# Optimization experiments

Hardware: AMD Instinct MI355X
Metric: run time of the kernel (lower is better)

The kernel has to match this reference:

```python
import jax, jax.numpy as jnp
import numpy as np

B = 32          # batch
IN_C = 8        # in_channels
OUT_C = 8       # out_channels
K = 3           # kernel_size
PAD = 1         # padding
STRIDE = 1
MC = 32         # manifold_channels
H = W = 512


def setup_inputs() -> dict:
    key = jax.random.key(0)
    ks = jax.random.split(key, 8)
    s = 0.05
    return {
        "q": jax.random.normal(ks[0], (B, 1, 8, 8), jnp.float32),
        "x": jax.random.normal(ks[1], (B, IN_C, H, W), jnp.float32),
        # manifold conv1: Conv2d(1, MC, 8) -> weight [MC,1,8,8], bias [MC]
        "wm1": jax.random.normal(ks[2], (MC, 1, 8, 8), jnp.float32) * s,
        "bm1": jax.random.normal(ks[3], (MC,), jnp.float32) * s,
        # manifold conv2: Conv2d(MC, MC, 1) -> stored as [MC_out, MC_in]
        "wm2": jax.random.normal(ks[4], (MC, MC), jnp.float32) * s,
        "bm2": jnp.zeros((MC,), jnp.float32),
        # weight_transform: ConvTranspose2d(MC, OUT_C*IN_C, K) -> [MC, OUT_C*IN_C, K, K]
        "wt": jax.random.normal(ks[5], (MC, OUT_C * IN_C, K, K), jnp.float32) * s,
        "bt": jnp.zeros((OUT_C * IN_C,), jnp.float32),
        # bias_transform: Conv2d(MC, OUT_C, 1) -> [OUT_C, MC]
        "wb": jax.random.normal(ks[6], (OUT_C, MC), jnp.float32) * s,
        "bb": jnp.zeros((OUT_C,), jnp.float32),
    }


def reference(q, x, wm1, bm1, wm2, bm2, wt, bt, wb, bb):
    # ---- manifold: Conv2d(1,MC,8) on 8x8 input == full contraction -> [B, MC]
    m = jnp.einsum('bihw,cihw->bc', q, wm1) + bm1
    m = jax.nn.leaky_relu(m)                      # torch default slope 0.01
    m = m @ wm2.T + bm2                           # 1x1 conv on 1x1 map
    m = jax.nn.leaky_relu(m)
    # ---- weight_transform: ConvTranspose2d from 1x1 input -> [B, OUT_C*IN_C, K, K]
    w = jnp.einsum('bc,cokl->bokl', m, wt) + bt[None, :, None, None]
    w = w.reshape(B, OUT_C, IN_C, K, K)           # per-sample conv filters
    # ---- bias_transform: 1x1 conv -> per-sample bias [B, OUT_C]
    b = m @ wb.T + bb
    # ---- per-sample conv2d (== grouped conv with groups=batch)
    def per_sample_conv(xi, wi):
        # xi: [IN_C, H, W], wi: [OUT_C, IN_C, K, K]
        return jax.lax.conv_general_dilated(
            xi[None], wi,
            window_strides=(STRIDE, STRIDE),
            padding=[(PAD, PAD), (PAD, PAD)],
            dimension_numbers=('NCHW', 'OIHW', 'NCHW'))[0]
    y = jax.vmap(per_sample_conv)(x, w)           # [B, OUT_C, H, W]
    y = y + b[:, :, None, None]
    return y
```

## Files before the change

### kernel.cpp

```cpp
#include <hip/hip_runtime.h>
#include <hip/hip_bf16.h>

#define B_    32
#define IN_C  8
#define OUT_C 8
#define KK    3
#define MC    32
#define HH_   512
#define WW_   512

__global__ __launch_bounds__(576) void manifold_kernel(
    const float* __restrict__ q, const float* __restrict__ wm1,
    const float* __restrict__ bm1, const float* __restrict__ wm2,
    const float* __restrict__ bm2, const float* __restrict__ wt,
    const float* __restrict__ bt, const float* __restrict__ wb,
    const float* __restrict__ bb, float* __restrict__ F,
    float* __restrict__ bS)
{
    __shared__ float m1s[MC];
    __shared__ float m2s[MC];
    const int b = blockIdx.x;
    const int t = threadIdx.x;

    if (t < MC) {
        float s = 0.f;
        #pragma unroll 8
        for (int j = 0; j < 64; ++j)
            s += q[b * 64 + j] * wm1[t * 64 + j];
        s += bm1[t];
        m1s[t] = (s > 0.f) ? s : 0.01f * s;
    }
    __syncthreads();
    if (t < MC) {
        float s2 = 0.f;
        #pragma unroll
        for (int k = 0; k < MC; ++k)
            s2 += m1s[k] * wm2[t * MC + k];
        s2 += bm2[t];
        m2s[t] = (s2 > 0.f) ? s2 : 0.01f * s2;
    }
    __syncthreads();

    {
        const int o   = t & 7;
        const int tap = t >> 3;
        const int i   = tap / 9;
        const int kk  = tap - i * 9;
        const int widx = (o * IN_C + i) * 9 + kk;
        float acc = bt[o * IN_C + i];
        #pragma unroll
        for (int cc = 0; cc < MC; ++cc)
            acc += m2s[cc] * wt[cc * 576 + widx];
        F[b * 576 + t] = acc;
    }

    if (t < OUT_C) {
        float acc = bb[t];
        #pragma unroll
        for (int cc = 0; cc < MC; ++cc)
            acc += m2s[cc] * wb[t * MC + cc];
        bS[b * OUT_C + t] = acc;
    }
}

#define PITCH 76

__global__ __launch_bounds__(256, 4) void conv_main_kernel(
    const float* __restrict__ x, const float* __restrict__ F,
    const float* __restrict__ bS, float* __restrict__ y)
{
    __shared__ float buf[4][18][PITCH];

    const int b  = blockIdx.z;
    const int w0 = blockIdx.x * 64;
    const int h0 = blockIdx.y * 16;
    const int tid = threadIdx.x;
    const int tx = tid & 15;
    const int ty = tid >> 4;
    const int h  = h0 + ty;
    const int w  = w0 + tx * 4;

    const float* __restrict__ Fb = F + b * 576;
    const float* __restrict__ xb = x + (size_t)b * IN_C * HH_ * WW_;

    float acc[OUT_C][4];
    #pragma unroll
    for (int o = 0; o < OUT_C; ++o) {
        float bv = bS[b * OUT_C + o];
        #pragma unroll
        for (int p = 0; p < 4; ++p) acc[o][p] = bv;
    }

    #pragma unroll
    for (int c4 = 0; c4 < 2; ++c4) {
        for (int idx = tid; idx < 4 * 18 * 18; idx += 256) {
            int ii  = idx / 324;
            int rem = idx - ii * 324;
            int rr  = rem / 18;
            int g   = rem - rr * 18;
            int hh   = h0 - 1 + rr;
            int gcol = w0 - 4 + 4 * g;
            float4 v = make_float4(0.f, 0.f, 0.f, 0.f);
            if ((unsigned)hh < (unsigned)HH_ && (unsigned)gcol < (unsigned)WW_) {
                const float* src = xb + ((size_t)(c4 * 4 + ii) * HH_ + hh) * WW_ + gcol;
                v = *reinterpret_cast<const float4*>(src);
            }
            *reinterpret_cast<float4*>(&buf[ii][rr][4 * g]) = v;
        }
        __syncthreads();

        #pragma unroll
        for (int ii = 0; ii < 4; ++ii) {
            const int i = c4 * 4 + ii;
            #pragma unroll
            for (int r = 0; r < KK; ++r) {
                const int rowr = ty + r;
                float4 xm = *reinterpret_cast<const float4*>(&buf[ii][rowr][4 * tx + 4]);
                float  xl = buf[ii][rowr][4 * tx + 3];
                float  xr = buf[ii][rowr][4 * tx + 8];
                float xv[6] = { xl, xm.x, xm.y, xm.z, xm.w, xr };
                #pragma unroll
                for (int kw = 0; kw < KK; ++kw) {
                    #pragma unroll
                    for (int o = 0; o < OUT_C; ++o) {
                        const float f = Fb[(i * 9 + r * 3 + kw) * 8 + o];
                        #pragma unroll
                        for (int p = 0; p < 4; ++p)
                            acc[o][p] += xv[kw + p] * f;
                    }
                }
            }
        }
        __syncthreads();
    }

    #pragma unroll
    for (int o = 0; o < OUT_C; ++o) {
        float4 v = make_float4(acc[o][0], acc[o][1], acc[o][2], acc[o][3]);
        float* yp = y + (((size_t)b * OUT_C + o) * HH_ + h) * WW_ + w;
        *reinterpret_cast<float4*>(yp) = v;
    }
}

extern "C" void kernel_launch(void* const* d_in, const int* in_sizes, int n_in,
                              void* d_out, int out_size, void* d_ws, size_t ws_size,
                              hipStream_t stream)
{
    const float* q   = (const float*)d_in[0];
    const float* x   = (const float*)d_in[1];
    const float* wm1 = (const float*)d_in[2];
    const float* bm1 = (const float*)d_in[3];
    const float* wm2 = (const float*)d_in[4];
    const float* bm2 = (const float*)d_in[5];
    const float* wt  = (const float*)d_in[6];
    const float* bt  = (const float*)d_in[7];
    const float* wb  = (const float*)d_in[8];
    const float* bb  = (const float*)d_in[9];
    float* out = (float*)d_out;

    float* Fw = (float*)d_ws;
    float* bS = Fw + B_ * 576;

    manifold_kernel<<<B_, 576, 0, stream>>>(q, wm1, bm1, wm2, bm2, wt, bt, wb, bb, Fw, bS);

    dim3 grid(WW_ / 64, HH_ / 16, B_);
    conv_main_kernel<<<grid, 256, 0, stream>>>(x, Fw, bS, out);
}
```

Before: 552.0 us.

## Replace LDS-staged input tiles with direct global loads in per-sample conv

Removes the shared-memory staging of input halo tiles and the block-wide barriers, and has each thread read its own three rows per input channel (a float4 plus two edge scalars) straight from global memory, relying on L1/L2 for reuse between neighbouring threads. The launch-bounds occupancy hint rises from 4 to 6 blocks per CU now that no LDS is used. This trades barrier and LDS traffic for more global and cache loads, some of them unaligned scalars.

Measured after the change: 1.543 ms. 179% more time.

```diff
diff --git a/kernel.cpp b/kernel.cpp
--- a/kernel.cpp
+++ b/kernel.cpp
@@ -63,14 +63,10 @@
     }
 }
 
-#define PITCH 76
-
-__global__ __launch_bounds__(256, 4) void conv_main_kernel(
+__global__ __launch_bounds__(256, 6) void conv_main_kernel(
     const float* __restrict__ x, const float* __restrict__ F,
     const float* __restrict__ bS, float* __restrict__ y)
 {
-    __shared__ float buf[4][18][PITCH];
-
     const int b  = blockIdx.z;
     const int w0 = blockIdx.x * 64;
     const int h0 = blockIdx.y * 16;
@@ -92,46 +88,34 @@
     }
 
     #pragma unroll
-    for (int c4 = 0; c4 < 2; ++c4) {
-        for (int idx = tid; idx < 4 * 18 * 18; idx += 256) {
-            int ii  = idx / 324;
-            int rem = idx - ii * 324;
-            int rr  = rem / 18;
-            int g   = rem - rr * 18;
-            int hh   = h0 - 1 + rr;
-            int gcol = w0 - 4 + 4 * g;
-            float4 v = make_float4(0.f, 0.f, 0.f, 0.f);
-            if ((unsigned)hh < (unsigned)HH_ && (unsigned)gcol < (unsigned)WW_) {
-                const float* src = xb + ((size_t)(c4 * 4 + ii) * HH_ + hh) * WW_ + gcol;
-                v = *reinterpret_cast<const float4*>(src);
+    for (int i = 0; i < IN_C; ++i) {
+        const float* __restrict__ xc = xb + (size_t)i * (HH_ * WW_);
+        #pragma unroll
+        for (int r = 0; r < KK; ++r) {
+            const int hh = h - 1 + r;
+            const bool rowok = ((unsigned)hh < (unsigned)HH_);
+            const float* rp = xc + (ptrdiff_t)hh * WW_ + w;
+
+            float4 xm = make_float4(0.f, 0.f, 0.f, 0.f);
+            float xl = 0.f, xr = 0.f;
+            if (rowok) {
+                xm = *reinterpret_cast<const float4*>(rp);
+                if (w > 0)            xl = rp[-1];
+                if (w + 4 < WW_)      xr = rp[4];
             }
-            *reinterpret_cast<float4*>(&buf[ii][rr][4 * g]) = v;
-        }
-        __syncthreads();
+            const float xv[6] = { xl, xm.x, xm.y, xm.z, xm.w, xr };
 
-        #pragma unroll
-        for (int ii = 0; ii < 4; ++ii) {
-            const int i = c4 * 4 + ii;
             #pragma unroll
-            for (int r = 0; r < KK; ++r) {
-                const int rowr = ty + r;
-                float4 xm = *reinterpret_cast<const float4*>(&buf[ii][rowr][4 * tx + 4]);
-                float  xl = buf[ii][rowr][4 * tx + 3];
-                float  xr = buf[ii][rowr][4 * tx + 8];
-                float xv[6] = { xl, xm.x, xm.y, xm.z, xm.w, xr };
+            for (int kw = 0; kw < KK; ++kw) {
                 #pragma unroll
-                for (int kw = 0; kw < KK; ++kw) {
+                for (int o = 0; o < OUT_C; ++o) {
+                    const float f = Fb[(i * 9 + r * 3 + kw) * 8 + o];
                     #pragma unroll
-                    for (int o = 0; o < OUT_C; ++o) {
-                        const float f = Fb[(i * 9 + r * 3 + kw) * 8 + o];
-                        #pragma unroll
-                        for (int p = 0; p < 4; ++p)
-                            acc[o][p] += xv[kw + p] * f;
-                    }
+                    for (int p = 0; p < 4; ++p)
+                        acc[o][p] += xv[kw + p] * f;
                 }
             }
         }
-        __syncthreads();
     }
 
     #pragma unroll
```
